# Kernel optimization log

Measured on AMD Instinct MI355X. Metric: run time of the kernel, lower is better.

The kernel has to match this reference:

```python
import jax, jax.numpy as jnp
import numpy as np

N = 50000      # nodes
E = 800000     # edges (before self-loops)
F = 128        # num_features
H = 64         # hidden_channels
B = 512        # batch_size (num graphs)
NC = 10        # num_classes


def setup_inputs() -> dict:
    key = jax.random.key(0)
    ks = jax.random.split(key, 24)
    rn = lambda k, shp, s=0.05: jax.random.normal(k, shp, jnp.float32) * s
    inp = {}
    inp["x"] = jax.random.normal(ks[0], (N, F), jnp.float32)
    inp["edge_index"] = jax.random.randint(ks[1], (2, E), 0, N)
    inp["batch"] = jnp.sort(jax.random.randint(ks[2], (N,), 0, B))
    # GATConv1: in F -> 4 heads x H (concat)
    inp["W1"] = rn(ks[3], (F, 4 * H)); inp["a_src1"] = rn(ks[4], (4, H))
    inp["a_dst1"] = rn(ks[5], (4, H)); inp["b1"] = rn(ks[6], (4 * H,))
    # GATConv2: in 4H -> 1 head x 2H
    inp["W2"] = rn(ks[7], (4 * H, 2 * H)); inp["a_src2"] = rn(ks[8], (1, 2 * H))
    inp["a_dst2"] = rn(ks[9], (1, 2 * H)); inp["b2"] = rn(ks[10], (2 * H,))
    # GCNConv: in 2H -> H
    inp["Wg"] = rn(ks[11], (2 * H, H)); inp["bg"] = rn(ks[12], (H,))
    # BatchNorms (eval mode: running_mean=0, running_var=1)
    inp["bn1_g"] = 1.0 + rn(ks[13], (4 * H,)); inp["bn1_b"] = rn(ks[14], (4 * H,))
    inp["bn2_g"] = 1.0 + rn(ks[15], (2 * H,)); inp["bn2_b"] = rn(ks[16], (2 * H,))
    inp["bn3_g"] = 1.0 + rn(ks[17], (2 * H,)); inp["bn3_b"] = rn(ks[18], (2 * H,))
    inp["lin1_W"] = rn(ks[19], (H, 128)); inp["lin1_b"] = rn(ks[20], (128,))
    inp["lin2_W"] = rn(ks[21], (128, NC)); inp["lin2_b"] = rn(ks[22], (NC,))
    inp["batch_size"] = B
    return inp


def _gat(x, src, dst, W, a_s, a_d, b, n):
    """PyG GATConv (eval): project, edge attention (leaky_relu 0.2), dst-softmax, scatter."""
    heads, ch = a_s.shape
    h = (x @ W).reshape(n, heads, ch)                       # [N, heads, ch]
    sc_s = (h * a_s).sum(-1)                                # [N, heads]
    sc_d = (h * a_d).sum(-1)
    e = jax.nn.leaky_relu(sc_s[src] + sc_d[dst], 0.2)       # [E2, heads]
    m = jax.ops.segment_max(e, dst, num_segments=n)
    ee = jnp.exp(e - m[dst])
    s = jax.ops.segment_sum(ee, dst, num_segments=n)
    alpha = ee / (s[dst] + 1e-16)                           # edge softmax per dst
    out = jax.ops.segment_sum(h[src] * alpha[:, :, None], dst, num_segments=n)
    return out.reshape(n, heads * ch) + b


def _bn_eval(x, g, b, eps=1e-5):
    # BatchNorm1d eval with running_mean=0, running_var=1
    return x * (g / jnp.sqrt(1.0 + eps)) + b


def reference(x, edge_index, batch, W1, a_src1, a_dst1, b1, W2, a_src2, a_dst2, b2,
              Wg, bg, bn1_g, bn1_b, bn2_g, bn2_b, bn3_g, bn3_b,
              lin1_W, lin1_b, lin2_W, lin2_b, batch_size):
    n = x.shape[0]
    loop = jnp.arange(n)
    src = jnp.concatenate([edge_index[0], loop])            # add self-loops (PyG default)
    dst = jnp.concatenate([edge_index[1], loop])
    lrelu = lambda v: jax.nn.leaky_relu(v, 0.01)            # module's LeakyReLU()

    x1 = _bn_eval(lrelu(_gat(x, src, dst, W1, a_src1, a_dst1, b1, n)), bn1_g, bn1_b)
    x2 = _bn_eval(lrelu(_gat(x1, src, dst, W2, a_src2, a_dst2, b2, n)), bn2_g, bn2_b)

    # GCNConv with symmetric normalization over A + I
    deg = jax.ops.segment_sum(jnp.ones_like(dst, jnp.float32), dst, num_segments=n)
    dis = jnp.where(deg > 0, jax.lax.rsqrt(deg), 0.0)
    h = x2 @ Wg                                             # [N, H]
    msg = h[src] * (dis[src] * dis[dst])[:, None]
    x3 = lrelu(jax.ops.segment_sum(msg, dst, num_segments=n) + bg)

    # global_mean_pool over graphs (dropout is identity in eval)
    sums = jax.ops.segment_sum(x3, batch, num_segments=batch_size)
    cnt = jax.ops.segment_sum(jnp.ones((n,), jnp.float32), batch, num_segments=batch_size)
    pooled = sums / jnp.clip(cnt, 1.0)[:, None]             # [B, H]

    y = lrelu(_bn_eval(pooled @ lin1_W + lin1_b, bn3_g, bn3_b))
    return y @ lin2_W + lin2_b                              # [B, NC]
```

## Files before the change

kernel.cpp:

```cpp
#include <hip/hip_runtime.h>
#include <hip/hip_bf16.h>

#define NN  50000
#define EE  800000
#define NE2 850000
#define NB  512
#define NRT 3125
#define NSB 196
#define NEB ((NE2 + 255) / 256)

#define BN_RS 0.9999950000374997f

typedef __attribute__((ext_vector_type(8))) short short8;
typedef __attribute__((ext_vector_type(4))) float f32x4;

__device__ __forceinline__ float bf2f(__hip_bfloat16 v) { return __bfloat162float(v); }
__device__ __forceinline__ unsigned short f2b(float v) {
    __hip_bfloat16 b = __float2bfloat16(v);
    return *reinterpret_cast<unsigned short*>(&b);
}
__device__ __forceinline__ float u2f(unsigned short u) {
    union { unsigned u; float f; } c; c.u = ((unsigned)u) << 16; return c.f;
}
__device__ __forceinline__ float lrelu01(float v) { return v > 0.f ? v : 0.01f * v; }
__device__ __forceinline__ float lrelu02(float v) { return v > 0.f ? v : 0.2f * v; }

__device__ __forceinline__ void up2(unsigned u, float& lo, float& hi) {
    union { unsigned x; float f; } a, b;
    a.x = u << 16; b.x = u & 0xFFFF0000u;
    lo = a.f; hi = b.f;
}
__device__ __forceinline__ void acc8(float* acc, uint4 u, float e) {
    float lo, hi;
    up2(u.x, lo, hi); acc[0] = fmaf(lo, e, acc[0]); acc[1] = fmaf(hi, e, acc[1]);
    up2(u.y, lo, hi); acc[2] = fmaf(lo, e, acc[2]); acc[3] = fmaf(hi, e, acc[3]);
    up2(u.z, lo, hi); acc[4] = fmaf(lo, e, acc[4]); acc[5] = fmaf(hi, e, acc[5]);
    up2(u.w, lo, hi); acc[6] = fmaf(lo, e, acc[6]); acc[7] = fmaf(hi, e, acc[7]);
}
__device__ __forceinline__ unsigned packbf2(float lo, float hi) {
    return ((unsigned)f2b(hi) << 16) | (unsigned)f2b(lo);
}

__device__ __forceinline__ void edge_sd(const int* __restrict__ ei, int e, int& s, int& d) {
    if (e < EE) { s = ei[e]; d = ei[EE + e]; }
    else        { s = e - EE; d = e - EE; }
}

__device__ __forceinline__ float ldf(const void* p, int i, bool bf) {
    return bf ? bf2f(((const __hip_bfloat16*)p)[i]) : ((const float*)p)[i];
}

#define NSEG 20
#define WTOT 85578
#define XQUADS (NN * 32)
#define PREP_TOT (NE2 + XQUADS + WTOT + 32768 + 32768 + 8192)
struct SegArgs { const void* src[NSEG]; int off[NSEG]; };

__global__ __launch_bounds__(256) void prep_k(SegArgs a,
                                              const void* __restrict__ x_raw,
                                              ushort4* __restrict__ xb4,
                                              const void* __restrict__ W1r,
                                              const void* __restrict__ W2r,
                                              const void* __restrict__ Wgr,
                                              float* __restrict__ wf,
                                              unsigned short* __restrict__ W1t,
                                              unsigned short* __restrict__ W2t,
                                              unsigned short* __restrict__ Wgt,
                                              const int* __restrict__ ei,
                                              int* __restrict__ degi,
                                              int* __restrict__ rank,
                                              int* __restrict__ flag) {
    __shared__ int cnt;
    int t = threadIdx.x;
    if (t == 0) cnt = 0;
    __syncthreads();
    {
        int c = 0;
        const unsigned* xw = (const unsigned*)x_raw;
#pragma unroll
        for (int k = 0; k < 4; ++k) {
            unsigned w = xw[t * 4 + k];
            unsigned ef = (w >> 7) & 0xFFu;
            if (ef >= 100u && ef <= 140u) c++;
        }
        atomicAdd(&cnt, c);
    }
    __syncthreads();
    bool bf = (cnt > 512);
    if (blockIdx.x == 0 && t == 0) *flag = bf ? 1 : 0;

    int i = blockIdx.x * 256 + t;
    if (i >= PREP_TOT) return;
    if (i < NE2) {
        int s, d; edge_sd(ei, i, s, d);
        rank[i] = atomicAdd(&degi[d], 1);
        return;
    }
    i -= NE2;
    if (i < XQUADS) {
        ushort4 o;
        if (bf) o = ((const ushort4*)x_raw)[i];
        else {
            float4 v = ((const float4*)x_raw)[i];
            o.x = f2b(v.x); o.y = f2b(v.y); o.z = f2b(v.z); o.w = f2b(v.w);
        }
        xb4[i] = o;
        return;
    }
    i -= XQUADS;
    if (i < WTOT) {
        int s = 0;
#pragma unroll
        for (int k = 1; k < NSEG; ++k) if (i >= a.off[k]) s = k;
        wf[i] = ldf(a.src[s], i - a.off[s], bf);
        return;
    }
    i -= WTOT;
    if (i < 32768) {
        int n = i >> 7, k = i & 127;
        W1t[i] = f2b(ldf(W1r, k * 256 + n, bf));
        return;
    }
    i -= 32768;
    if (i < 32768) {
        int n = i >> 8, k = i & 255;
        W2t[i] = f2b(ldf(W2r, k * 128 + n, bf));
        return;
    }
    i -= 32768;
    {
        int n = i >> 7, k = i & 127;
        Wgt[i] = f2b(ldf(Wgr, k * 64 + n, bf));
    }
}

__global__ __launch_bounds__(256) void pscan_k(const int* __restrict__ degi,
                                               int* __restrict__ incl, int* __restrict__ bsum) {
    __shared__ int tmp[256];
    int t = threadIdx.x;
    int i = blockIdx.x * 256 + t;
    int v = (i < NN) ? degi[i] : 0;
    tmp[t] = v;
    __syncthreads();
#pragma unroll
    for (int off = 1; off < 256; off <<= 1) {
        int u = (t >= off) ? tmp[t - off] : 0;
        __syncthreads();
        tmp[t] += u;
        __syncthreads();
    }
    if (i < NN) incl[i] = tmp[t];
    if (t == 255) bsum[blockIdx.x] = tmp[255];
}

__global__ __launch_bounds__(256) void bscan_k(int* __restrict__ bsum) {
    __shared__ int tmp[256];
    int t = threadIdx.x;
    tmp[t] = (t < NSB) ? bsum[t] : 0;
    __syncthreads();
#pragma unroll
    for (int off = 1; off < 256; off <<= 1) {
        int u = (t >= off) ? tmp[t - off] : 0;
        __syncthreads();
        tmp[t] += u;
        __syncthreads();
    }
    if (t < NSB) bsum[t] = tmp[t];
}

__global__ __launch_bounds__(256) void fscan_k(const int* __restrict__ degi,
                                               const int* __restrict__ incl,
                                               const int* __restrict__ bsum,
                                               const int* __restrict__ batch,
                                               int* __restrict__ row_ptr,
                                               float* __restrict__ dis, int* __restrict__ gstart) {
    int i = blockIdx.x * 256 + threadIdx.x;
    if (i <= NB) {
        int lo = 0, hi = NN;
        while (lo < hi) { int mid = (lo + hi) >> 1; if (batch[mid] < i) lo = mid + 1; else hi = mid; }
        gstart[i] = lo;
    }
    if (i >= NN) return;
    int dg = degi[i];
    int base = (blockIdx.x > 0) ? bsum[blockIdx.x - 1] : 0;
    int ex = base + incl[i] - dg;
    row_ptr[i] = ex;
    dis[i] = dg > 0 ? rsqrtf((float)dg) : 0.f;
    if (i == NN - 1) row_ptr[NN] = bsum[NSB - 1];
}

__global__ __launch_bounds__(256) void scatter_k(const int* __restrict__ ei,
                                                 const int* __restrict__ row_ptr,
                                                 const int* __restrict__ rank,
                                                 int* __restrict__ csr_src) {
    int e = blockIdx.x * 256 + threadIdx.x;
    if (e >= NE2) return;
    int s, d; edge_sd(ei, e, s, d);
    csr_src[row_ptr[d] + rank[e]] = s;
}

__global__ __launch_bounds__(256) void mgemm1_k(const short* __restrict__ A,
                                                const short* __restrict__ Bt,
                                                unsigned short* __restrict__ C,
                                                const float* __restrict__ a_s,
                                                const float* __restrict__ a_d,
                                                float* __restrict__ sc_s,
                                                float* __restrict__ sc_d) {
    int wave = threadIdx.x >> 6, lane = threadIdx.x & 63;
    int cg = wave;
    int l15 = lane & 15, quad = lane >> 4;
    const short* bp = Bt + (size_t)(cg * 64 + l15) * 128 + quad * 8;
    short8 bfr[4][4];
#pragma unroll
    for (int j = 0; j < 4; ++j)
#pragma unroll
        for (int kk = 0; kk < 4; ++kk)
            bfr[j][kk] = *(const short8*)(bp + (size_t)j * 16 * 128 + kk * 32);
    float asv[4], adv[4];
#pragma unroll
    for (int j = 0; j < 4; ++j) {
        asv[j] = a_s[cg * 64 + j * 16 + l15];
        adv[j] = a_d[cg * 64 + j * 16 + l15];
    }
#pragma unroll
    for (int rtl = 0; rtl < 4; ++rtl) {
        int rt = blockIdx.x * 4 + rtl;
        if (rt >= NRT) break;
        const short* ap = A + (size_t)(rt * 16 + l15) * 128 + quad * 8;
        f32x4 acc[4] = {};
#pragma unroll
        for (int kk = 0; kk < 4; ++kk) {
            short8 a = *(const short8*)(ap + kk * 32);
#pragma unroll
            for (int j = 0; j < 4; ++j)
                acc[j] = __builtin_amdgcn_mfma_f32_16x16x32_bf16(a, bfr[j][kk], acc[j], 0, 0, 0);
        }
        float ss[4] = {0.f, 0.f, 0.f, 0.f}, sd[4] = {0.f, 0.f, 0.f, 0.f};
#pragma unroll
        for (int j = 0; j < 4; ++j) {
            int n = cg * 64 + j * 16 + l15;
#pragma unroll
            for (int r = 0; r < 4; ++r) {
                float v = acc[j][r];
                C[(size_t)(rt * 16 + quad * 4 + r) * 256 + n] = f2b(v);
                ss[r] = fmaf(v, asv[j], ss[r]);
                sd[r] = fmaf(v, adv[j], sd[r]);
            }
        }
#pragma unroll
        for (int off = 1; off < 16; off <<= 1) {
#pragma unroll
            for (int r = 0; r < 4; ++r) {
                ss[r] += __shfl_xor(ss[r], off);
                sd[r] += __shfl_xor(sd[r], off);
            }
        }
        if (l15 == 0) {
#pragma unroll
            for (int r = 0; r < 4; ++r) {
                int node = rt * 16 + quad * 4 + r;
                sc_s[node * 4 + cg] = ss[r];
                sc_d[node * 4 + cg] = sd[r];
            }
        }
    }
}

__global__ __launch_bounds__(256) void mgemm2_k(const short* __restrict__ A,
                                                const short* __restrict__ Bt,
                                                unsigned short* __restrict__ C,
                                                const float* __restrict__ a_s,
                                                const float* __restrict__ a_d,
                                                float* __restrict__ sc_s,
                                                float* __restrict__ sc_d) {
    __shared__ float sred[4][16][2];
    int wave = threadIdx.x >> 6, lane = threadIdx.x & 63;
    int gidx = blockIdx.x * 4 + wave;
    bool act = gidx < NRT * 2;
    int gcl = act ? gidx : NRT * 2 - 1;
    int rt = gcl >> 1, cg = gcl & 1;
    int l15 = lane & 15, quad = lane >> 4;
    const short* ap = A + (size_t)(rt * 16 + l15) * 256 + quad * 8;
    const short* bp = Bt + (size_t)(cg * 64 + l15) * 256 + quad * 8;
    f32x4 acc[4] = {};
    for (int k0 = 0; k0 < 256; k0 += 32) {
        short8 a = *(const short8*)(ap + k0);
#pragma unroll
        for (int j = 0; j < 4; ++j) {
            short8 b = *(const short8*)(bp + (size_t)j * 16 * 256 + k0);
            acc[j] = __builtin_amdgcn_mfma_f32_16x16x32_bf16(a, b, acc[j], 0, 0, 0);
        }
    }
    float asv[4], adv[4];
#pragma unroll
    for (int j = 0; j < 4; ++j) {
        asv[j] = a_s[cg * 64 + j * 16 + l15];
        adv[j] = a_d[cg * 64 + j * 16 + l15];
    }
    float ss[4] = {0.f, 0.f, 0.f, 0.f}, sd[4] = {0.f, 0.f, 0.f, 0.f};
#pragma unroll
    for (int j = 0; j < 4; ++j) {
        int n = cg * 64 + j * 16 + l15;
#pragma unroll
        for (int r = 0; r < 4; ++r) {
            float v = acc[j][r];
            if (act) C[(size_t)(rt * 16 + quad * 4 + r) * 128 + n] = f2b(v);
            ss[r] = fmaf(v, asv[j], ss[r]);
            sd[r] = fmaf(v, adv[j], sd[r]);
        }
    }
#pragma unroll
    for (int off = 1; off < 16; off <<= 1) {
#pragma unroll
        for (int r = 0; r < 4; ++r) {
            ss[r] += __shfl_xor(ss[r], off);
            sd[r] += __shfl_xor(sd[r], off);
        }
    }
    if (l15 == 0) {
#pragma unroll
        for (int r = 0; r < 4; ++r) {
            sred[wave][quad * 4 + r][0] = ss[r];
            sred[wave][quad * 4 + r][1] = sd[r];
        }
    }
    __syncthreads();
    if (threadIdx.x < 32) {
        int rl = threadIdx.x >> 4, row = threadIdx.x & 15;
        int g2 = blockIdx.x * 4 + rl * 2;
        if (g2 < NRT * 2) {
            int node = (g2 >> 1) * 16 + row;
            sc_s[node] = sred[rl * 2][row][0] + sred[rl * 2 + 1][row][0];
            sc_d[node] = sred[rl * 2][row][1] + sred[rl * 2 + 1][row][1];
        }
    }
}

__global__ __launch_bounds__(256) void mgemm3_k(const short* __restrict__ A,
                                                const short* __restrict__ Bt,
                                                unsigned short* __restrict__ C) {
    int wave = threadIdx.x >> 6, lane = threadIdx.x & 63;
    int wt = blockIdx.x * 4 + wave;
    int l15 = lane & 15, quad = lane >> 4;
    const short* bp = Bt + (size_t)l15 * 128 + quad * 8;
    short8 bfr[4][4];
#pragma unroll
    for (int j = 0; j < 4; ++j)
#pragma unroll
        for (int kk = 0; kk < 4; ++kk)
            bfr[j][kk] = *(const short8*)(bp + (size_t)j * 16 * 128 + kk * 32);
#pragma unroll
    for (int rtl = 0; rtl < 4; ++rtl) {
        int rt = wt * 4 + rtl;
        if (rt >= NRT) break;
        const short* ap = A + (size_t)(rt * 16 + l15) * 128 + quad * 8;
        f32x4 acc[4] = {};
#pragma unroll
        for (int kk = 0; kk < 4; ++kk) {
            short8 a = *(const short8*)(ap + kk * 32);
#pragma unroll
            for (int j = 0; j < 4; ++j)
                acc[j] = __builtin_amdgcn_mfma_f32_16x16x32_bf16(a, bfr[j][kk], acc[j], 0, 0, 0);
        }
#pragma unroll
        for (int j = 0; j < 4; ++j) {
            int n = j * 16 + l15;
#pragma unroll
            for (int r = 0; r < 4; ++r)
                C[(size_t)(rt * 16 + quad * 4 + r) * 64 + n] = f2b(acc[j][r]);
        }
    }
}

__device__ __forceinline__ float sel4(float4 v, int head) {
    float ab = (head & 1) ? v.y : v.x;
    float cd = (head & 1) ? v.w : v.z;
    return (head & 2) ? cd : ab;
}

__global__ __launch_bounds__(256) void agg1_k(const int* __restrict__ row_ptr,
                                              const int* __restrict__ csr_src,
                                              const uint4* __restrict__ h1b,
                                              const float* __restrict__ sc_s,
                                              const float4* __restrict__ sc_d4,
                                              const float4* __restrict__ b1,
                                              const float4* __restrict__ g1,
                                              const float4* __restrict__ bb1,
                                              uint4* __restrict__ x1b) {
    int n = __builtin_amdgcn_readfirstlane((blockIdx.x * 256 + threadIdx.x) >> 6);
    int lane = threadIdx.x & 63;
    if (n >= NN) return;
    int g = lane >> 5, sl = lane & 31;
    int head = sl >> 3;
    int row = row_ptr[n], end = row_ptr[n + 1];
    float scd_h = sel4(sc_d4[n], head);
    float acc[8] = {0.f, 0.f, 0.f, 0.f, 0.f, 0.f, 0.f, 0.f};
    float den = 0.f;
    int c = row;
    for (; c + 7 < end; c += 8) {
        int i0 = c + g, i1 = c + 2 + g, i2 = c + 4 + g, i3 = c + 6 + g;
        int s0 = csr_src[i0], s1 = csr_src[i1], s2 = csr_src[i2], s3 = csr_src[i3];
        float w0 = sc_s[s0 * 4 + head], w1 = sc_s[s1 * 4 + head];
        float w2 = sc_s[s2 * 4 + head], w3 = sc_s[s3 * 4 + head];
        uint4 u0 = h1b[(size_t)s0 * 32 + sl];
        uint4 u1 = h1b[(size_t)s1 * 32 + sl];
        uint4 u2 = h1b[(size_t)s2 * 32 + sl];
        uint4 u3 = h1b[(size_t)s3 * 32 + sl];
        float e0 = __expf(lrelu02(w0 + scd_h));
        float e1 = __expf(lrelu02(w1 + scd_h));
        float e2 = __expf(lrelu02(w2 + scd_h));
        float e3 = __expf(lrelu02(w3 + scd_h));
        den += (e0 + e1) + (e2 + e3);
        acc8(acc, u0, e0); acc8(acc, u1, e1); acc8(acc, u2, e2); acc8(acc, u3, e3);
    }
    if (c < end) {
        int i0 = c + g, i1 = c + 2 + g, i2 = c + 4 + g, i3 = c + 6 + g;
        bool v0 = i0 < end, v1 = i1 < end, v2 = i2 < end, v3 = i3 < end;
        int l = end - 1;
        int s0 = csr_src[v0 ? i0 : l], s1 = csr_src[v1 ? i1 : l];
        int s2 = csr_src[v2 ? i2 : l], s3 = csr_src[v3 ? i3 : l];
        float w0 = sc_s[s0 * 4 + head], w1 = sc_s[s1 * 4 + head];
        float w2 = sc_s[s2 * 4 + head], w3 = sc_s[s3 * 4 + head];
        uint4 u0 = h1b[(size_t)s0 * 32 + sl];
        uint4 u1 = h1b[(size_t)s1 * 32 + sl];
        uint4 u2 = h1b[(size_t)s2 * 32 + sl];
        uint4 u3 = h1b[(size_t)s3 * 32 + sl];
        float e0 = v0 ? __expf(lrelu02(w0 + scd_h)) : 0.f;
        float e1 = v1 ? __expf(lrelu02(w1 + scd_h)) : 0.f;
        float e2 = v2 ? __expf(lrelu02(w2 + scd_h)) : 0.f;
        float e3 = v3 ? __expf(lrelu02(w3 + scd_h)) : 0.f;
        den += (e0 + e1) + (e2 + e3);
        acc8(acc, u0, e0); acc8(acc, u1, e1); acc8(acc, u2, e2); acc8(acc, u3, e3);
    }
    den += __shfl_xor(den, 32);
#pragma unroll
    for (int k = 0; k < 8; ++k) acc[k] += __shfl_xor(acc[k], 32);
    if (g == 0) {
        float inv = 1.f / (den + 1e-16f);
        float4 bA = b1[sl * 2],  bB = b1[sl * 2 + 1];
        float4 gA = g1[sl * 2],  gB = g1[sl * 2 + 1];
        float4 eA = bb1[sl * 2], eB = bb1[sl * 2 + 1];
        float o0 = lrelu01(fmaf(acc[0], inv, bA.x)) * (gA.x * BN_RS) + eA.x;
        float o1 = lrelu01(fmaf(acc[1], inv, bA.y)) * (gA.y * BN_RS) + eA.y;
        float o2 = lrelu01(fmaf(acc[2], inv, bA.z)) * (gA.z * BN_RS) + eA.z;
        float o3 = lrelu01(fmaf(acc[3], inv, bA.w)) * (gA.w * BN_RS) + eA.w;
        float o4 = lrelu01(fmaf(acc[4], inv, bB.x)) * (gB.x * BN_RS) + eB.x;
        float o5 = lrelu01(fmaf(acc[5], inv, bB.y)) * (gB.y * BN_RS) + eB.y;
        float o6 = lrelu01(fmaf(acc[6], inv, bB.z)) * (gB.z * BN_RS) + eB.z;
        float o7 = lrelu01(fmaf(acc[7], inv, bB.w)) * (gB.w * BN_RS) + eB.w;
        uint4 w;
        w.x = packbf2(o0, o1); w.y = packbf2(o2, o3);
        w.z = packbf2(o4, o5); w.w = packbf2(o6, o7);
        x1b[(size_t)n * 32 + sl] = w;
    }
}

__global__ __launch_bounds__(256) void agg2_k(const int* __restrict__ row_ptr,
                                              const int* __restrict__ csr_src,
                                              const uint4* __restrict__ h2b,
                                              const float* __restrict__ sc_s,
                                              const float* __restrict__ sc_d,
                                              const float4* __restrict__ b2,
                                              const float4* __restrict__ g2,
                                              const float4* __restrict__ bb2,
                                              uint4* __restrict__ x2b) {
    int n = __builtin_amdgcn_readfirstlane((blockIdx.x * 256 + threadIdx.x) >> 6);
    int lane = threadIdx.x & 63;
    if (n >= NN) return;
    int g = lane >> 4, sl = lane & 15;
    int row = row_ptr[n], end = row_ptr[n + 1];
    float scd = sc_d[n];
    float acc[8] = {0.f, 0.f, 0.f, 0.f, 0.f, 0.f, 0.f, 0.f};
    float den = 0.f;
    int c = row;
    for (; c + 15 < end; c += 16) {
        int i0 = c + g, i1 = c + 4 + g, i2 = c + 8 + g, i3 = c + 12 + g;
        int s0 = csr_src[i0], s1 = csr_src[i1], s2 = csr_src[i2], s3 = csr_src[i3];
        float c0 = sc_s[s0], c1 = sc_s[s1], c2 = sc_s[s2], c3 = sc_s[s3];
        uint4 u0 = h2b[(size_t)s0 * 16 + sl];
        uint4 u1 = h2b[(size_t)s1 * 16 + sl];
        uint4 u2 = h2b[(size_t)s2 * 16 + sl];
        uint4 u3 = h2b[(size_t)s3 * 16 + sl];
        float e0 = __expf(lrelu02(c0 + scd));
        float e1 = __expf(lrelu02(c1 + scd));
        float e2 = __expf(lrelu02(c2 + scd));
        float e3 = __expf(lrelu02(c3 + scd));
        den += (e0 + e1) + (e2 + e3);
        acc8(acc, u0, e0); acc8(acc, u1, e1); acc8(acc, u2, e2); acc8(acc, u3, e3);
    }
    if (c < end) {
        int i0 = c + g, i1 = c + 4 + g, i2 = c + 8 + g, i3 = c + 12 + g;
        bool v0 = i0 < end, v1 = i1 < end, v2 = i2 < end, v3 = i3 < end;
        int l = end - 1;
        int s0 = csr_src[v0 ? i0 : l], s1 = csr_src[v1 ? i1 : l];
        int s2 = csr_src[v2 ? i2 : l], s3 = csr_src[v3 ? i3 : l];
        float c0 = sc_s[s0], c1 = sc_s[s1], c2 = sc_s[s2], c3 = sc_s[s3];
        uint4 u0 = h2b[(size_t)s0 * 16 + sl];
        uint4 u1 = h2b[(size_t)s1 * 16 + sl];
        uint4 u2 = h2b[(size_t)s2 * 16 + sl];
        uint4 u3 = h2b[(size_t)s3 * 16 + sl];
        float e0 = v0 ? __expf(lrelu02(c0 + scd)) : 0.f;
        float e1 = v1 ? __expf(lrelu02(c1 + scd)) : 0.f;
        float e2 = v2 ? __expf(lrelu02(c2 + scd)) : 0.f;
        float e3 = v3 ? __expf(lrelu02(c3 + scd)) : 0.f;
        den += (e0 + e1) + (e2 + e3);
        acc8(acc, u0, e0); acc8(acc, u1, e1); acc8(acc, u2, e2); acc8(acc, u3, e3);
    }
    den += __shfl_xor(den, 16);
    den += __shfl_xor(den, 32);
#pragma unroll
    for (int k = 0; k < 8; ++k) {
        acc[k] += __shfl_xor(acc[k], 16);
        acc[k] += __shfl_xor(acc[k], 32);
    }
    if (lane < 16) {
        float inv = 1.f / (den + 1e-16f);
        float4 bA = b2[sl * 2],  bB = b2[sl * 2 + 1];
        float4 gA = g2[sl * 2],  gB = g2[sl * 2 + 1];
        float4 eA = bb2[sl * 2], eB = bb2[sl * 2 + 1];
        float o0 = lrelu01(fmaf(acc[0], inv, bA.x)) * (gA.x * BN_RS) + eA.x;
        float o1 = lrelu01(fmaf(acc[1], inv, bA.y)) * (gA.y * BN_RS) + eA.y;
        float o2 = lrelu01(fmaf(acc[2], inv, bA.z)) * (gA.z * BN_RS) + eA.z;
        float o3 = lrelu01(fmaf(acc[3], inv, bA.w)) * (gA.w * BN_RS) + eA.w;
        float o4 = lrelu01(fmaf(acc[4], inv, bB.x)) * (gB.x * BN_RS) + eB.x;
        float o5 = lrelu01(fmaf(acc[5], inv, bB.y)) * (gB.y * BN_RS) + eB.y;
        float o6 = lrelu01(fmaf(acc[6], inv, bB.z)) * (gB.z * BN_RS) + eB.z;
        float o7 = lrelu01(fmaf(acc[7], inv, bB.w)) * (gB.w * BN_RS) + eB.w;
        uint4 w;
        w.x = packbf2(o0, o1); w.y = packbf2(o2, o3);
        w.z = packbf2(o4, o5); w.w = packbf2(o6, o7);
        x2b[(size_t)n * 16 + sl] = w;
    }
}

__global__ __launch_bounds__(256) void gcn_k(const int* __restrict__ row_ptr,
                                             const int* __restrict__ csr_src,
                                             const uint4* __restrict__ hgb,
                                             const float* __restrict__ dis,
                                             const float4* __restrict__ bg,
                                             float4* __restrict__ x3) {
    int n = __builtin_amdgcn_readfirstlane((blockIdx.x * 256 + threadIdx.x) >> 6);
    int lane = threadIdx.x & 63;
    if (n >= NN) return;
    int g = lane >> 3, sl = lane & 7;
    int row = row_ptr[n], end = row_ptr[n + 1];
    float dn = dis[n];
    float acc[8] = {0.f, 0.f, 0.f, 0.f, 0.f, 0.f, 0.f, 0.f};
    int c = row;
    for (; c + 15 < end; c += 16) {
        int i0 = c + g, i1 = c + 8 + g;
        int s0 = csr_src[i0], s1 = csr_src[i1];
        float w0 = dis[s0], w1 = dis[s1];
        uint4 u0 = hgb[(size_t)s0 * 8 + sl];
        uint4 u1 = hgb[(size_t)s1 * 8 + sl];
        acc8(acc, u0, w0); acc8(acc, u1, w1);
    }
    if (c < end) {
        int i0 = c + g, i1 = c + 8 + g;
        bool v0 = i0 < end, v1 = i1 < end;
        int l = end - 1;
        int s0 = csr_src[v0 ? i0 : l], s1 = csr_src[v1 ? i1 : l];
        float w0 = v0 ? dis[s0] : 0.f, w1 = v1 ? dis[s1] : 0.f;
        uint4 u0 = hgb[(size_t)s0 * 8 + sl];
        uint4 u1 = hgb[(size_t)s1 * 8 + sl];
        acc8(acc, u0, w0); acc8(acc, u1, w1);
    }
#pragma unroll
    for (int off = 8; off <= 32; off <<= 1) {
#pragma unroll
        for (int k = 0; k < 8; ++k) acc[k] += __shfl_xor(acc[k], off);
    }
    if (lane < 8) {
        float4 bA = bg[sl * 2], bB = bg[sl * 2 + 1];
        float4 oA, oB;
        oA.x = lrelu01(fmaf(acc[0], dn, bA.x));
        oA.y = lrelu01(fmaf(acc[1], dn, bA.y));
        oA.z = lrelu01(fmaf(acc[2], dn, bA.z));
        oA.w = lrelu01(fmaf(acc[3], dn, bA.w));
        oB.x = lrelu01(fmaf(acc[4], dn, bB.x));
        oB.y = lrelu01(fmaf(acc[5], dn, bB.y));
        oB.z = lrelu01(fmaf(acc[6], dn, bB.z));
        oB.w = lrelu01(fmaf(acc[7], dn, bB.w));
        x3[(size_t)n * 16 + sl * 2]     = oA;
        x3[(size_t)n * 16 + sl * 2 + 1] = oB;
    }
}

__global__ __launch_bounds__(256) void poolmlp_k(const float* __restrict__ x3,
                                                 const int* __restrict__ gstart,
                                                 const float* __restrict__ l1W,
                                                 const float* __restrict__ l1b,
                                                 const float* __restrict__ g3,
                                                 const float* __restrict__ b3,
                                                 const float* __restrict__ l2W,
                                                 const float* __restrict__ l2b,
                                                 void* __restrict__ outp,
                                                 const int* __restrict__ flag) {
    __shared__ float red[4][64];
    __shared__ float pl[64];
    __shared__ float y1s[128];
    int g = blockIdx.x, t = threadIdx.x;
    int c = t & 63, r = t >> 6;
    int s = gstart[g], e = gstart[g + 1];
    float sum = 0.f;
    for (int n = s + r; n < e; n += 4) sum += x3[(size_t)n * 64 + c];
    red[r][c] = sum;
    __syncthreads();
    if (t < 64) {
        float v = red[0][t] + red[1][t] + red[2][t] + red[3][t];
        int cnt = e - s; if (cnt < 1) cnt = 1;
        pl[t] = v / (float)cnt;
    }
    __syncthreads();
    if (t < 128) {
        float acc = l1b[t];
#pragma unroll 8
        for (int j = 0; j < 64; ++j) acc = fmaf(pl[j], l1W[j * 128 + t], acc);
        acc = acc * (g3[t] * BN_RS) + b3[t];
        y1s[t] = lrelu01(acc);
    }
    __syncthreads();
    if (t < 10) {
        float o = l2b[t];
#pragma unroll 8
        for (int j = 0; j < 128; ++j) o = fmaf(y1s[j], l2W[j * 10 + t], o);
        if (*flag) ((__hip_bfloat16*)outp)[g * 10 + t] = __float2bfloat16(o);
        else       ((float*)outp)[g * 10 + t] = o;
    }
}

static const int kSegN[NSEG]  = {32768, 256, 256, 256, 32768, 128, 128, 128, 8192, 64,
                                 256, 256, 128, 128, 128, 128, 8192, 128, 1280, 10};
static const int kSegIn[NSEG] = {3, 4, 5, 6, 7, 8, 9, 10, 11, 12, 13, 14, 15, 16, 17, 18, 19, 20, 21, 22};

extern "C" void kernel_launch(void* const* d_in, const int* in_sizes, int n_in,
                              void* d_out, int out_size, void* d_ws, size_t ws_size,
                              hipStream_t stream) {
    const void* x_raw = d_in[0];
    const int*  ei    = (const int*)d_in[1];
    const int*  batch = (const int*)d_in[2];

    int*   flag = (int*)d_ws;
    float* ws   = (float*)d_ws;
    unsigned short* xb = (unsigned short*)(ws + 16);
    float* wf   = ws + 16 + (size_t)NN * 64;
    unsigned short* W1t = (unsigned short*)(wf + 85584);
    unsigned short* W2t = W1t + 32768;
    unsigned short* Wgt = W2t + 32768;
    unsigned short* h1b = Wgt + 8192;
    unsigned short* x1b = h1b + (size_t)NN * 256;
    unsigned short* x2b = x1b + (size_t)NN * 256;
    unsigned short* hgb = x2b + (size_t)NN * 128;
    float* x3   = (float*)(hgb + (size_t)NN * 64);
    float* sc_s1 = x3 + (size_t)NN * 64;
    float* sc_d1 = sc_s1 + (size_t)NN * 4;
    float* sc_s2 = sc_d1 + (size_t)NN * 4;
    float* sc_d2 = sc_s2 + NN;
    float* disb  = sc_d2 + NN;
    int*   gstart = (int*)(disb + NN);
    int*   degi   = gstart + NB + 4;
    int*   incl   = degi + NN;
    int*   bsum   = incl + NN;
    int*   row_ptr = bsum + 256;
    int*   cursor  = row_ptr + NN + 1;
    int*   csr_src = cursor + NN;

    int*   rankb = (int*)x1b;

    int off[NSEG]; int o = 0;
    for (int s = 0; s < NSEG; ++s) { off[s] = o; o += kSegN[s]; }
    float* as1f = wf + off[1];  float* ad1f = wf + off[2];
    float* b1f  = wf + off[3];  float* as2f = wf + off[5];
    float* ad2f = wf + off[6];  float* b2f  = wf + off[7];
    float* bgf  = wf + off[9];  float* bn1g = wf + off[10]; float* bn1b = wf + off[11];
    float* bn2g = wf + off[12]; float* bn2b = wf + off[13]; float* bn3g = wf + off[14];
    float* bn3b = wf + off[15]; float* l1Wf = wf + off[16]; float* l1bf = wf + off[17];
    float* l2Wf = wf + off[18]; float* l2bf = wf + off[19];

    unsigned short* h2b = h1b;

    hipMemsetAsync(degi, 0, NN * sizeof(int), stream);
    SegArgs sa;
    for (int s = 0; s < NSEG; ++s) { sa.src[s] = d_in[kSegIn[s]]; sa.off[s] = off[s]; }
    prep_k<<<(PREP_TOT + 255) / 256, 256, 0, stream>>>(sa, x_raw, (ushort4*)xb,
                                                       d_in[3], d_in[7], d_in[11],
                                                       wf, W1t, W2t, Wgt, ei, degi, rankb, flag);

    pscan_k<<<NSB, 256, 0, stream>>>(degi, incl, bsum);
    bscan_k<<<1, 256, 0, stream>>>(bsum);
    fscan_k<<<NSB, 256, 0, stream>>>(degi, incl, bsum, batch, row_ptr, disb, gstart);
    scatter_k<<<NEB, 256, 0, stream>>>(ei, row_ptr, rankb, csr_src);

    mgemm1_k<<<(NRT + 3) / 4, 256, 0, stream>>>((const short*)xb, (const short*)W1t, h1b,
                                                as1f, ad1f, sc_s1, sc_d1);
    agg1_k<<<12500, 256, 0, stream>>>(row_ptr, csr_src, (const uint4*)h1b,
                                      sc_s1, (const float4*)sc_d1,
                                      (const float4*)b1f, (const float4*)bn1g,
                                      (const float4*)bn1b, (uint4*)x1b);

    mgemm2_k<<<(NRT * 2 + 3) / 4, 256, 0, stream>>>((const short*)x1b, (const short*)W2t, h2b,
                                                    as2f, ad2f, sc_s2, sc_d2);
    agg2_k<<<12500, 256, 0, stream>>>(row_ptr, csr_src, (const uint4*)h2b,
                                      sc_s2, sc_d2,
                                      (const float4*)b2f, (const float4*)bn2g,
                                      (const float4*)bn2b, (uint4*)x2b);

    mgemm3_k<<<(NRT + 15) / 16, 256, 0, stream>>>((const short*)x2b, (const short*)Wgt, hgb);
    gcn_k<<<12500, 256, 0, stream>>>(row_ptr, csr_src, (const uint4*)hgb, disb,
                                     (const float4*)bgf, (float4*)x3);
    poolmlp_k<<<NB, 256, 0, stream>>>(x3, gstart, l1Wf, l1bf, bn3g, bn3b, l2Wf, l2bf,
                                      d_out, flag);
}
```

Baseline: 384.5 us.

## Fuse CSR build scans and scatter into one cooperative kernel; store x3 in bf16

Replaces the four CSR-construction kernels (block scan, block-sum scan, finalize, scatter) with a single cooperative-groups kernel that uses grid.sync between phases, removing three launches and the incl intermediate buffer. Each block recomputes its base offset by reducing the preceding block sums. Separately, the GCN output x3 is stored as bf16 instead of fp32, halving the bytes written by gcn_k and read by poolmlp_k, with some precision loss in pooling inputs. Cooperative launch needs all 196 blocks co-resident and the scatter becomes a grid-stride loop over fewer threads.

```diff
diff --git a/kernel.cpp b/kernel.cpp
--- a/kernel.cpp
+++ b/kernel.cpp
@@ -1,5 +1,8 @@
 #include <hip/hip_runtime.h>
 #include <hip/hip_bf16.h>
+#include <hip/hip_cooperative_groups.h>
+
+namespace cg = cooperative_groups;
 
 #define NN  50000
 #define EE  800000
@@ -7,7 +10,6 @@
 #define NB  512
 #define NRT 3125
 #define NSB 196
-#define NEB ((NE2 + 255) / 256)
 
 #define BN_RS 0.9999950000374997f
 
@@ -134,11 +136,19 @@
     }
 }
 
-__global__ __launch_bounds__(256) void pscan_k(const int* __restrict__ degi,
-                                               int* __restrict__ incl, int* __restrict__ bsum) {
+__global__ __launch_bounds__(256) void csr_k(const int* __restrict__ degi,
+                                             const int* __restrict__ ei,
+                                             const int* __restrict__ batch,
+                                             const int* __restrict__ rank,
+                                             int* __restrict__ bsum,
+                                             int* __restrict__ row_ptr,
+                                             float* __restrict__ dis,
+                                             int* __restrict__ gstart,
+                                             int* __restrict__ csr_src) {
+    cg::grid_group grid = cg::this_grid();
     __shared__ int tmp[256];
-    int t = threadIdx.x;
-    int i = blockIdx.x * 256 + t;
+    int t = threadIdx.x, b = blockIdx.x;
+    int i = b * 256 + t;
     int v = (i < NN) ? degi[i] : 0;
     tmp[t] = v;
     __syncthreads();
@@ -149,54 +159,35 @@
         tmp[t] += u;
         __syncthreads();
     }
-    if (i < NN) incl[i] = tmp[t];
-    if (t == 255) bsum[blockIdx.x] = tmp[255];
-}
-
-__global__ __launch_bounds__(256) void bscan_k(int* __restrict__ bsum) {
-    __shared__ int tmp[256];
-    int t = threadIdx.x;
-    tmp[t] = (t < NSB) ? bsum[t] : 0;
-    __syncthreads();
-#pragma unroll
-    for (int off = 1; off < 256; off <<= 1) {
-        int u = (t >= off) ? tmp[t - off] : 0;
+    int incl = tmp[t];
+    if (t == 255) bsum[b] = tmp[255];
+    grid.sync();
+    int x = (t < NSB && t < b) ? bsum[t] : 0;
+    __syncthreads();
+    tmp[t] = x;
+    __syncthreads();
+#pragma unroll
+    for (int off = 128; off > 0; off >>= 1) {
+        if (t < off) tmp[t] += tmp[t + off];
         __syncthreads();
-        tmp[t] += u;
-        __syncthreads();
-    }
-    if (t < NSB) bsum[t] = tmp[t];
-}
-
-__global__ __launch_bounds__(256) void fscan_k(const int* __restrict__ degi,
-                                               const int* __restrict__ incl,
-                                               const int* __restrict__ bsum,
-                                               const int* __restrict__ batch,
-                                               int* __restrict__ row_ptr,
-                                               float* __restrict__ dis, int* __restrict__ gstart) {
-    int i = blockIdx.x * 256 + threadIdx.x;
+    }
+    int base = tmp[0];
+    int ex = base + incl - v;
+    if (i < NN) {
+        row_ptr[i] = ex;
+        dis[i] = v > 0 ? rsqrtf((float)v) : 0.f;
+        if (i == NN - 1) row_ptr[NN] = ex + v;
+    }
     if (i <= NB) {
         int lo = 0, hi = NN;
         while (lo < hi) { int mid = (lo + hi) >> 1; if (batch[mid] < i) lo = mid + 1; else hi = mid; }
         gstart[i] = lo;
     }
-    if (i >= NN) return;
-    int dg = degi[i];
-    int base = (blockIdx.x > 0) ? bsum[blockIdx.x - 1] : 0;
-    int ex = base + incl[i] - dg;
-    row_ptr[i] = ex;
-    dis[i] = dg > 0 ? rsqrtf((float)dg) : 0.f;
-    if (i == NN - 1) row_ptr[NN] = bsum[NSB - 1];
-}
-
-__global__ __launch_bounds__(256) void scatter_k(const int* __restrict__ ei,
-                                                 const int* __restrict__ row_ptr,
-                                                 const int* __restrict__ rank,
-                                                 int* __restrict__ csr_src) {
-    int e = blockIdx.x * 256 + threadIdx.x;
-    if (e >= NE2) return;
-    int s, d; edge_sd(ei, e, s, d);
-    csr_src[row_ptr[d] + rank[e]] = s;
+    grid.sync();
+    for (int e = i; e < NE2; e += NSB * 256) {
+        int s, d; edge_sd(ei, e, s, d);
+        csr_src[row_ptr[d] + rank[e]] = s;
+    }
 }
 
 __global__ __launch_bounds__(256) void mgemm1_k(const short* __restrict__ A,
@@ -207,9 +198,9 @@
                                                 float* __restrict__ sc_s,
                                                 float* __restrict__ sc_d) {
     int wave = threadIdx.x >> 6, lane = threadIdx.x & 63;
-    int cg = wave;
+    int cg2 = wave;
     int l15 = lane & 15, quad = lane >> 4;
-    const short* bp = Bt + (size_t)(cg * 64 + l15) * 128 + quad * 8;
+    const short* bp = Bt + (size_t)(cg2 * 64 + l15) * 128 + quad * 8;
     short8 bfr[4][4];
 #pragma unroll
     for (int j = 0; j < 4; ++j)
@@ -219,8 +210,8 @@
     float asv[4], adv[4];
 #pragma unroll
     for (int j = 0; j < 4; ++j) {
-        asv[j] = a_s[cg * 64 + j * 16 + l15];
-        adv[j] = a_d[cg * 64 + j * 16 + l15];
+        asv[j] = a_s[cg2 * 64 + j * 16 + l15];
+        adv[j] = a_d[cg2 * 64 + j * 16 + l15];
     }
 #pragma unroll
     for (int rtl = 0; rtl < 4; ++rtl) {
@@ -238,7 +229,7 @@
         float ss[4] = {0.f, 0.f, 0.f, 0.f}, sd[4] = {0.f, 0.f, 0.f, 0.f};
 #pragma unroll
         for (int j = 0; j < 4; ++j) {
-            int n = cg * 64 + j * 16 + l15;
+            int n = cg2 * 64 + j * 16 + l15;
 #pragma unroll
             for (int r = 0; r < 4; ++r) {
                 float v = acc[j][r];
@@ -259,8 +250,8 @@
 #pragma unroll
             for (int r = 0; r < 4; ++r) {
                 int node = rt * 16 + quad * 4 + r;
-                sc_s[node * 4 + cg] = ss[r];
-                sc_d[node * 4 + cg] = sd[r];
+                sc_s[node * 4 + cg2] = ss[r];
+                sc_d[node * 4 + cg2] = sd[r];
             }
         }
     }
@@ -278,10 +269,10 @@
     int gidx = blockIdx.x * 4 + wave;
     bool act = gidx < NRT * 2;
     int gcl = act ? gidx : NRT * 2 - 1;
-    int rt = gcl >> 1, cg = gcl & 1;
+    int rt = gcl >> 1, cg2 = gcl & 1;
     int l15 = lane & 15, quad = lane >> 4;
     const short* ap = A + (size_t)(rt * 16 + l15) * 256 + quad * 8;
-    const short* bp = Bt + (size_t)(cg * 64 + l15) * 256 + quad * 8;
+    const short* bp = Bt + (size_t)(cg2 * 64 + l15) * 256 + quad * 8;
     f32x4 acc[4] = {};
     for (int k0 = 0; k0 < 256; k0 += 32) {
         short8 a = *(const short8*)(ap + k0);
@@ -294,13 +285,13 @@
     float asv[4], adv[4];
 #pragma unroll
     for (int j = 0; j < 4; ++j) {
-        asv[j] = a_s[cg * 64 + j * 16 + l15];
-        adv[j] = a_d[cg * 64 + j * 16 + l15];
+        asv[j] = a_s[cg2 * 64 + j * 16 + l15];
+        adv[j] = a_d[cg2 * 64 + j * 16 + l15];
     }
     float ss[4] = {0.f, 0.f, 0.f, 0.f}, sd[4] = {0.f, 0.f, 0.f, 0.f};
 #pragma unroll
     for (int j = 0; j < 4; ++j) {
-        int n = cg * 64 + j * 16 + l15;
+        int n = cg2 * 64 + j * 16 + l15;
 #pragma unroll
         for (int r = 0; r < 4; ++r) {
             float v = acc[j][r];
@@ -538,7 +529,7 @@
                                              const uint4* __restrict__ hgb,
                                              const float* __restrict__ dis,
                                              const float4* __restrict__ bg,
-                                             float4* __restrict__ x3) {
+                                             uint4* __restrict__ x3b) {
     int n = __builtin_amdgcn_readfirstlane((blockIdx.x * 256 + threadIdx.x) >> 6);
     int lane = threadIdx.x & 63;
     if (n >= NN) return;
@@ -572,21 +563,22 @@
     }
     if (lane < 8) {
         float4 bA = bg[sl * 2], bB = bg[sl * 2 + 1];
-        float4 oA, oB;
-        oA.x = lrelu01(fmaf(acc[0], dn, bA.x));
-        oA.y = lrelu01(fmaf(acc[1], dn, bA.y));
-        oA.z = lrelu01(fmaf(acc[2], dn, bA.z));
-        oA.w = lrelu01(fmaf(acc[3], dn, bA.w));
-        oB.x = lrelu01(fmaf(acc[4], dn, bB.x));
-        oB.y = lrelu01(fmaf(acc[5], dn, bB.y));
-        oB.z = lrelu01(fmaf(acc[6], dn, bB.z));
-        oB.w = lrelu01(fmaf(acc[7], dn, bB.w));
-        x3[(size_t)n * 16 + sl * 2]     = oA;
-        x3[(size_t)n * 16 + sl * 2 + 1] = oB;
-    }
-}
-
-__global__ __launch_bounds__(256) void poolmlp_k(const float* __restrict__ x3,
+        float o0 = lrelu01(fmaf(acc[0], dn, bA.x));
+        float o1 = lrelu01(fmaf(acc[1], dn, bA.y));
+        float o2 = lrelu01(fmaf(acc[2], dn, bA.z));
+        float o3 = lrelu01(fmaf(acc[3], dn, bA.w));
+        float o4 = lrelu01(fmaf(acc[4], dn, bB.x));
+        float o5 = lrelu01(fmaf(acc[5], dn, bB.y));
+        float o6 = lrelu01(fmaf(acc[6], dn, bB.z));
+        float o7 = lrelu01(fmaf(acc[7], dn, bB.w));
+        uint4 w;
+        w.x = packbf2(o0, o1); w.y = packbf2(o2, o3);
+        w.z = packbf2(o4, o5); w.w = packbf2(o6, o7);
+        x3b[(size_t)n * 8 + sl] = w;
+    }
+}
+
+__global__ __launch_bounds__(256) void poolmlp_k(const unsigned short* __restrict__ x3b,
                                                  const int* __restrict__ gstart,
                                                  const float* __restrict__ l1W,
                                                  const float* __restrict__ l1b,
@@ -603,7 +595,7 @@
     int c = t & 63, r = t >> 6;
     int s = gstart[g], e = gstart[g + 1];
     float sum = 0.f;
-    for (int n = s + r; n < e; n += 4) sum += x3[(size_t)n * 64 + c];
+    for (int n = s + r; n < e; n += 4) sum += u2f(x3b[(size_t)n * 64 + c]);
     red[r][c] = sum;
     __syncthreads();
     if (t < 64) {
@@ -651,19 +643,17 @@
     unsigned short* x1b = h1b + (size_t)NN * 256;
     unsigned short* x2b = x1b + (size_t)NN * 256;
     unsigned short* hgb = x2b + (size_t)NN * 128;
-    float* x3   = (float*)(hgb + (size_t)NN * 64);
-    float* sc_s1 = x3 + (size_t)NN * 64;
+    unsigned short* x3b = hgb + (size_t)NN * 64;
+    float* sc_s1 = (float*)(x3b + (size_t)NN * 64);
     float* sc_d1 = sc_s1 + (size_t)NN * 4;
     float* sc_s2 = sc_d1 + (size_t)NN * 4;
     float* sc_d2 = sc_s2 + NN;
     float* disb  = sc_d2 + NN;
     int*   gstart = (int*)(disb + NN);
     int*   degi   = gstart + NB + 4;
-    int*   incl   = degi + NN;
-    int*   bsum   = incl + NN;
+    int*   bsum   = degi + NN;
     int*   row_ptr = bsum + 256;
-    int*   cursor  = row_ptr + NN + 1;
-    int*   csr_src = cursor + NN;
+    int*   csr_src = row_ptr + NN + 4;
 
     int*   rankb = (int*)x1b;
 
@@ -686,10 +676,14 @@
                                                        d_in[3], d_in[7], d_in[11],
                                                        wf, W1t, W2t, Wgt, ei, degi, rankb, flag);
 
-    pscan_k<<<NSB, 256, 0, stream>>>(degi, incl, bsum);
-    bscan_k<<<1, 256, 0, stream>>>(bsum);
-    fscan_k<<<NSB, 256, 0, stream>>>(degi, incl, bsum, batch, row_ptr, disb, gstart);
-    scatter_k<<<NEB, 256, 0, stream>>>(ei, row_ptr, rankb, csr_src);
+    {
+        const int* degi_c = degi; const int* ei_c = ei; const int* batch_c = batch;
+        const int* rank_c = rankb;
+        void* args[] = {(void*)&degi_c, (void*)&ei_c, (void*)&batch_c, (void*)&rank_c,
+                        (void*)&bsum, (void*)&row_ptr, (void*)&disb, (void*)&gstart,
+                        (void*)&csr_src};
+        hipLaunchCooperativeKernel((void*)csr_k, dim3(NSB), dim3(256), args, 0, stream);
+    }
 
     mgemm1_k<<<(NRT + 3) / 4, 256, 0, stream>>>((const short*)xb, (const short*)W1t, h1b,
                                                 as1f, ad1f, sc_s1, sc_d1);
@@ -707,7 +701,7 @@
 
     mgemm3_k<<<(NRT + 15) / 16, 256, 0, stream>>>((const short*)x2b, (const short*)Wgt, hgb);
     gcn_k<<<12500, 256, 0, stream>>>(row_ptr, csr_src, (const uint4*)hgb, disb,
-                                     (const float4*)bgf, (float4*)x3);
-    poolmlp_k<<<NB, 256, 0, stream>>>(x3, gstart, l1Wf, l1bf, bn3g, bn3b, l2Wf, l2bf,
+                                     (const float4*)bgf, (uint4*)x3b);
+    poolmlp_k<<<NB, 256, 0, stream>>>(x3b, gstart, l1Wf, l1bf, bn3g, bn3b, l2Wf, l2bf,
                                       d_out, flag);
 }
```

Result: slower. 458.7 us (+19.3%).
